# Kernel optimization log

Hardware: AMD Instinct MI355X
Metric: run time of the kernel (lower is better)

The kernel has to match this reference:

```python
import jax, jax.numpy as jnp
import numpy as np

S, B, D, H, DH = 1024, 4, 1024, 16, 64


def setup_inputs() -> dict:
    key = jax.random.key(0)
    ks = jax.random.split(key, 12)
    inp = {
        "query": jax.random.normal(ks[0], (S, B, D), dtype=jnp.float32),
        "key": jax.random.normal(ks[1], (S, B, D), dtype=jnp.float32),
        "value": jax.random.normal(ks[2], (S, B, D), dtype=jnp.float32),
        "key_mask": jax.random.randint(ks[3], (S, B), 0, 2, dtype=jnp.int32),
        # per-head stacked projection weights (original loops nn.Linear per head)
        "Wq": jax.random.normal(ks[4], (H, D, DH), dtype=jnp.float32) * 0.02,
        "bq": jnp.zeros((H, DH), dtype=jnp.float32),
        "Wk": jax.random.normal(ks[5], (H, D, DH), dtype=jnp.float32) * 0.02,
        "bk": jnp.zeros((H, DH), dtype=jnp.float32),
        "Wv": jax.random.normal(ks[6], (H, D, DH), dtype=jnp.float32) * 0.02,
        "bv": jnp.zeros((H, DH), dtype=jnp.float32),
        "Wo": jax.random.normal(ks[7], (H * DH, D), dtype=jnp.float32) * 0.02,
        "bo": jnp.zeros((D,), dtype=jnp.float32),
    }
    return inp


def reference(query, key, value, key_mask, Wq, bq, Wk, bk, Wv, bv, Wo, bo):
    # query/key/value: [S, B, D] (seq-major, matching torch einsum 'imk,jmk->imj')
    q = jnp.einsum('smd,hdk->smhk', query, Wq) + bq  # [Sq, B, H, DH]
    k = jnp.einsum('smd,hdk->smhk', key, Wk) + bk    # [Sk, B, H, DH]
    v = jnp.einsum('smd,hdk->smhk', value, Wv) + bv  # [Sk, B, H, DH]

    scale = 1.0 / jnp.sqrt(jnp.float32(DH))
    scores = jnp.einsum('imhk,jmhk->himj', q, k) * scale  # [H, Sq, B, Sk]
    # key_mask: [Sk, B] -> transpose -> [B, Sk]; additive -1e18 masking
    scores = scores - key_mask.astype(jnp.float32).T * 1e18
    attn = jax.nn.softmax(scores, axis=-1)
    out = jnp.einsum('himj,jmhk->imhk', attn, v)  # [Sq, B, H, DH]
    concat = out.reshape(out.shape[0], out.shape[1], H * DH)
    return concat @ Wo + bo  # [Sq, B, D]
```

## Files before the change

kernel.cpp:

```cpp
#include <hip/hip_runtime.h>
#include <hip/hip_bf16.h>


typedef __attribute__((ext_vector_type(8))) short short8;
typedef __attribute__((ext_vector_type(4))) short short4_;
typedef __attribute__((ext_vector_type(4))) float f32x4;
typedef __attribute__((ext_vector_type(16))) float f32x16;
typedef __attribute__((ext_vector_type(8))) __bf16 bf16x8;
typedef __attribute__((ext_vector_type(4))) __bf16 bf16x4;

union B8 {
    short8 s;
    bf16x8 b;
    unsigned short u[8];
};
union B4 {
    short4_ s;
    bf16x4 b;
    unsigned short u[4];
    int i[2];
};

#if __has_builtin(__builtin_amdgcn_exp2f)
#define EXP2(x) __builtin_amdgcn_exp2f(x)
#else
#define EXP2(x) exp2f(x)
#endif
#if __has_builtin(__builtin_amdgcn_rcpf)
#define RCP(x) __builtin_amdgcn_rcpf(x)
#else
#define RCP(x) (1.0f / (x))
#endif

static __device__ __forceinline__ unsigned short f2bf_rne(float f) {
    union { float f; unsigned u; } v; v.f = f;
    unsigned r = v.u + 0x7FFFu + ((v.u >> 16) & 1u);
    return (unsigned short)(r >> 16);
}

static __device__ __forceinline__ void async_lds16(const void* g, const void* l) {
    __builtin_amdgcn_global_load_lds(
        (const __attribute__((address_space(1))) unsigned int*)(unsigned long long)g,
        (__attribute__((address_space(3))) unsigned int*)(unsigned int)(unsigned long long)l,
        16, 0, 0);
}

__global__ __launch_bounds__(256) void prep(
    const float* __restrict__ Wq, const float* __restrict__ Wk,
    const float* __restrict__ Wv, const float* __restrict__ Wo,
    const float* __restrict__ query, const float* __restrict__ key,
    const float* __restrict__ value,
    unsigned short* __restrict__ WT,
    unsigned short* __restrict__ qA, unsigned short* __restrict__ kA,
    unsigned short* __restrict__ vA) {
    const int t = threadIdx.x;
    const int z = blockIdx.z;

    if (z >= 4) {
        const int zz = z - 4;
        const int tensor = zz >> 2;
        const int part = zz & 3;
        const float* src = (tensor == 0) ? query : (tensor == 1) ? key : value;
        unsigned short* dst = (tensor == 0) ? qA : (tensor == 1) ? kA : vA;
        const int blk = blockIdx.y * 16 + blockIdx.x;
        const size_t base = (size_t)part * 1048576 + (size_t)blk * 4096 + t * 16;
        B8 w0, w1;
#pragma unroll
        for (int i = 0; i < 2; ++i) {
            f32x4 a = *(const f32x4*)(src + base + i * 8);
            f32x4 b = *(const f32x4*)(src + base + i * 8 + 4);
#pragma unroll
            for (int j = 0; j < 4; ++j) {
                (i ? w1 : w0).u[j] = f2bf_rne(a[j]);
                (i ? w1 : w0).u[4 + j] = f2bf_rne(b[j]);
            }
        }
        *(short8*)(dst + base) = w0.s;
        *(short8*)(dst + base + 8) = w1.s;
        return;
    }

    __shared__ float sT[64][65];
    const int dtile = blockIdx.x;
    const int sub = blockIdx.y;
    const float* src;
    int spitch;
    unsigned short* dst;
    if (z < 3) {
        const float* W = (z == 0) ? Wq : (z == 1) ? Wk : Wv;
        src = W + (size_t)sub * 65536 + (size_t)dtile * 64 * 64;
        spitch = 64;
        dst = WT + (size_t)z * 1048576 + (size_t)(sub * 64) * 1024 + dtile * 64;
    } else {
        src = Wo + (size_t)dtile * 64 * 1024 + sub * 64;
        spitch = 1024;
        dst = WT + (size_t)3 * 1048576 + (size_t)(sub * 64) * 1024 + dtile * 64;
    }

    const int r = t >> 2;
    const int cseg = (t & 3) * 16;
#pragma unroll
    for (int i = 0; i < 4; ++i) {
        f32x4 v = *(const f32x4*)(src + (size_t)r * spitch + cseg + i * 4);
#pragma unroll
        for (int j = 0; j < 4; ++j) sT[r][cseg + i * 4 + j] = v[j];
    }
    __syncthreads();
    B8 w0, w1;
#pragma unroll
    for (int i = 0; i < 8; ++i) {
        w0.u[i] = f2bf_rne(sT[cseg + i][r]);
        w1.u[i] = f2bf_rne(sT[cseg + 8 + i][r]);
    }
    *(short8*)(dst + (size_t)r * 1024 + cseg) = w0.s;
    *(short8*)(dst + (size_t)r * 1024 + cseg + 8) = w1.s;
}

template <bool OUT_F32, bool BIAS_ROW>
__device__ __forceinline__ void gemm128(unsigned short* __restrict__ sA,
                                        unsigned short* __restrict__ sB,
                                        const unsigned short* __restrict__ A,
                                        size_t lda,
                                        const unsigned short* __restrict__ Bt,
                                        size_t ldb,
                                        const float* __restrict__ bias,
                                        void* __restrict__ Cv, size_t ldc,
                                        float oscale, int row0, int col0) {
    const int t = threadIdx.x;
    const int w = t >> 6;
    const int lane = t & 63;
    const int quad = lane >> 4;
    const int l15 = lane & 15;
    const int l7 = l15 & 7;
    const int wr = w >> 1;
    const int wc = w & 1;
    const int lrow8 = lane >> 3;
    const int lseg = lane & 7;
    const int gseg = lseg ^ lrow8;

    f32x4 acc[4][4] = {};

    for (int k0 = 0; k0 < 1024; k0 += 64) {
#pragma unroll
        for (int i = 0; i < 4; ++i) {
            const int rr = w * 32 + i * 8;
            async_lds16(A + (size_t)(row0 + rr + lrow8) * lda + k0 + gseg * 8,
                        &sA[rr * 64]);
            async_lds16(Bt + (size_t)(col0 + rr + lrow8) * ldb + k0 + gseg * 8,
                        &sB[rr * 64]);
        }
        __syncthreads();
#pragma unroll
        for (int kf = 0; kf < 2; ++kf) {
            B8 af[4], bf[4];
#pragma unroll
            for (int i = 0; i < 4; ++i)
                af[i].s = *(const short8*)&sA[(wr * 64 + i * 16 + l15) * 64 +
                                              ((kf * 4 + quad) ^ l7) * 8];
#pragma unroll
            for (int j = 0; j < 4; ++j)
                bf[j].s = *(const short8*)&sB[(wc * 64 + j * 16 + l15) * 64 +
                                              ((kf * 4 + quad) ^ l7) * 8];
#pragma unroll
            for (int i = 0; i < 4; ++i)
#pragma unroll
                for (int j = 0; j < 4; ++j)
                    acc[i][j] = __builtin_amdgcn_mfma_f32_16x16x32_bf16(af[i].b, bf[j].b,
                                                                        acc[i][j], 0, 0, 0);
        }
        __syncthreads();
    }
    float brow[4][4];
    if constexpr (BIAS_ROW) {
#pragma unroll
        for (int i = 0; i < 4; ++i)
#pragma unroll
            for (int r = 0; r < 4; ++r)
                brow[i][r] = bias[row0 + wr * 64 + i * 16 + quad * 4 + r];
    }
#pragma unroll
    for (int j = 0; j < 4; ++j) {
        const int col = col0 + wc * 64 + j * 16 + l15;
        const float bcol = BIAS_ROW ? 0.0f : bias[col];
#pragma unroll
        for (int i = 0; i < 4; ++i) {
#pragma unroll
            for (int r = 0; r < 4; ++r) {
                const int row = row0 + wr * 64 + i * 16 + quad * 4 + r;
                const size_t idx = (size_t)row * ldc + col;
                const float bb = BIAS_ROW ? brow[i][r] : bcol;
                const float val = (acc[i][j][r] + bb) * oscale;
                if constexpr (OUT_F32)
                    ((float*)Cv)[idx] = val;
                else
                    ((unsigned short*)Cv)[idx] = f2bf_rne(val);
            }
        }
    }
}

#define SCALE_L2E 0.18033688011112042f

__global__ __launch_bounds__(256) void qkv_gemm(
    const unsigned short* __restrict__ qA, const unsigned short* __restrict__ kA,
    const unsigned short* __restrict__ vA,
    const unsigned short* __restrict__ WT,
    const float* __restrict__ bq, const float* __restrict__ bk, const float* __restrict__ bv,
    unsigned short* q_o, unsigned short* k_o, unsigned short* vT_o) {
    __shared__ unsigned short sA[128 * 64];
    __shared__ unsigned short sB[128 * 64];
    const int p = blockIdx.z;
    if (p < 2) {
        const unsigned short* A = (p == 0) ? qA : kA;
        const unsigned short* Bt = WT + (size_t)p * 1048576;
        const float* bias = (p == 0) ? bq : bk;
        unsigned short* C = (p == 0) ? q_o : k_o;
        const float osc = (p == 0) ? SCALE_L2E : 1.0f;
        gemm128<false, false>(sA, sB, A, 1024, Bt, 1024, bias, C, 1024, osc,
                              blockIdx.x * 128, blockIdx.y * 128);
    } else {
        const int b = blockIdx.x >> 3;
        const int rt = blockIdx.x & 7;
        gemm128<false, true>(sA, sB, WT + (size_t)2 * 1048576, 1024,
                             vA + (size_t)b * 1024, 4096, bv,
                             vT_o + (size_t)b * 1048576, 1024, 1.0f,
                             rt * 128, blockIdx.y * 128);
    }
}

__global__ __launch_bounds__(256) void out_gemm(const unsigned short* __restrict__ A,
                                                const unsigned short* __restrict__ WT,
                                                const float* __restrict__ bo,
                                                float* __restrict__ C) {
    __shared__ unsigned short sA[128 * 64];
    __shared__ unsigned short sB[128 * 64];
    gemm128<true, false>(sA, sB, A, 1024, WT + (size_t)3 * 1048576, 1024, bo, C, 1024,
                         1.0f, blockIdx.x * 128, blockIdx.y * 128);
}

#define TP 72

#if __has_builtin(__builtin_amdgcn_mfma_f32_32x32x8bf16_1k)
#define HAVE_X8 1
#endif

__global__ __launch_bounds__(256) void attn_kernel(
    const unsigned short* __restrict__ q,
    const unsigned short* __restrict__ k,
    const unsigned short* __restrict__ vT,
    const int* __restrict__ key_mask,
    unsigned short* __restrict__ o) {
    __shared__ unsigned short sK[2][64 * TP];
    __shared__ unsigned short sVt[2][64 * TP];
    __shared__ float sBias[1024];
    __shared__ unsigned long long sBits[16];

    const int t = threadIdx.x;
    const int wave = t >> 6;
    const int lane = t & 63;
    const int n31 = lane & 31;
    const int hh = lane >> 5;

    const int L = blockIdx.x + 8 * (blockIdx.y + 4 * blockIdx.z);
    const int xcd = L & 7;
    const int kk = L >> 3;
    const int g = (xcd << 3) | (kk >> 3);
    const int qt = kk & 7;
    const int b = g & 3;
    const int h = g >> 2;
    const int q0w = qt * 128 + wave * 32;

    const int srow = t >> 3;
    const int sseg = t & 7;

#pragma unroll
    for (int i = 0; i < 4; ++i) {
        const int idx = i * 4 + wave;
        const int sk = idx * 64 + lane;
        unsigned long long bal = __ballot(key_mask[sk * 4 + b] != 0);
        if (lane == 0) sBits[idx] = bal;
    }
    __syncthreads();
#pragma unroll
    for (int i = 0; i < 4; ++i) {
        const int idx = t * 4 + i;
        const int r = idx & 15;
        const int hb = (idx >> 4) & 1;
        const int blk = (idx >> 5) & 1;
        const int kt = idx >> 6;
        const int row = (r & 3) + 8 * (r >> 2) + 4 * hb + blk * 32;
        sBias[idx] = ((sBits[kt] >> row) & 1ull) ? -16384.0f : 0.0f;
    }

    bf16x8 qf[4];
    {
        const unsigned short* qrow =
            q + ((size_t)(q0w + n31) * 4 + b) * 1024 + h * 64 + hh * 8;
#pragma unroll
        for (int kc = 0; kc < 4; ++kc) {
            B8 tmp;
            tmp.s = *(const short8*)(qrow + kc * 16);
            qf[kc] = tmp.b;
        }
    }

    f32x16 O0 = {}, O1 = {}, L_ = {};
    B4 ones;
#pragma unroll
    for (int j = 0; j < 4; ++j) ones.u[j] = 0x3F80;
#if !defined(HAVE_X8)
    B8 ones8;
#pragma unroll
    for (int j = 0; j < 8; ++j) ones8.u[j] = 0x3F80;
#endif

    const unsigned short* kbase = k + (size_t)b * 1024 + h * 64;
    const unsigned short* vtb = vT + ((size_t)(b * 16 + h) * 64) * 1024;

    {
        const unsigned short* kr = kbase + (size_t)srow * 4096 + sseg * 8;
        short8 ka = *(const short8*)kr;
        short8 kb2 = *(const short8*)(kr + (size_t)32 * 4096);
        const unsigned short* vr = vtb + (size_t)srow * 1024 + sseg * 8;
        short8 va = *(const short8*)vr;
        short8 vb2 = *(const short8*)(vr + (size_t)32 * 1024);
        *(short8*)&sK[0][srow * TP + sseg * 8] = ka;
        *(short8*)&sK[0][(32 + srow) * TP + sseg * 8] = kb2;
        *(short8*)&sVt[0][srow * TP + sseg * 8] = va;
        *(short8*)&sVt[0][(32 + srow) * TP + sseg * 8] = vb2;
    }

#pragma unroll 2
    for (int kt = 0; kt < 16; ++kt) {
        const int cur = kt & 1;
        __syncthreads();
        short8 nka, nkb, nva, nvb;
        if (kt < 15) {
            const int k0n = (kt + 1) * 64;
            const unsigned short* kr = kbase + (size_t)(k0n + srow) * 4096 + sseg * 8;
            nka = *(const short8*)kr;
            nkb = *(const short8*)(kr + (size_t)32 * 4096);
            const unsigned short* vr = vtb + (size_t)srow * 1024 + k0n + sseg * 8;
            nva = *(const short8*)vr;
            nvb = *(const short8*)(vr + (size_t)32 * 1024);
        }
        B4 pfr[2][4];
#pragma unroll
        for (int blk = 0; blk < 2; ++blk) {
            f32x16 c;
            const f32x4* bp = (const f32x4*)&sBias[((kt * 2 + blk) * 2 + hh) * 16];
#pragma unroll
            for (int i = 0; i < 4; ++i) {
                f32x4 x = bp[i];
#pragma unroll
                for (int j = 0; j < 4; ++j) c[i * 4 + j] = x[j];
            }
            __builtin_amdgcn_s_setprio(1);
#pragma unroll
            for (int kc = 0; kc < 4; ++kc) {
                B8 af;
                af.s = *(const short8*)&sK[cur][(blk * 32 + n31) * TP + kc * 16 + hh * 8];
                c = __builtin_amdgcn_mfma_f32_32x32x16_bf16(af.b, qf[kc], c, 0, 0, 0);
            }
            __builtin_amdgcn_s_setprio(0);
#pragma unroll
            for (int gg = 0; gg < 4; ++gg)
#pragma unroll
                for (int j = 0; j < 4; ++j)
                    pfr[blk][gg].b[j] = (__bf16)EXP2(c[gg * 4 + j]);
        }
#if defined(HAVE_X8)
        __builtin_amdgcn_s_setprio(1);
#pragma unroll
        for (int blk = 0; blk < 2; ++blk) {
#pragma unroll
            for (int gg = 0; gg < 4; ++gg) {
                const int sko = blk * 32 + gg * 8 + hh * 4;
                B4 b0, b1;
                b0.s = *(const short4_*)&sVt[cur][n31 * TP + sko];
                b1.s = *(const short4_*)&sVt[cur][(32 + n31) * TP + sko];
                O0 = __builtin_amdgcn_mfma_f32_32x32x8bf16_1k(pfr[blk][gg].s, b0.s, O0, 0, 0, 0);
                O1 = __builtin_amdgcn_mfma_f32_32x32x8bf16_1k(pfr[blk][gg].s, b1.s, O1, 0, 0, 0);
                L_ = __builtin_amdgcn_mfma_f32_32x32x8bf16_1k(pfr[blk][gg].s, ones.s, L_, 0, 0, 0);
            }
        }
        __builtin_amdgcn_s_setprio(0);
#else
        __builtin_amdgcn_s_setprio(1);
#pragma unroll
        for (int blk = 0; blk < 2; ++blk) {
            B4 par[4];
#pragma unroll
            for (int gg = 0; gg < 4; ++gg) {
                par[gg].i[0] = __shfl_xor(pfr[blk][gg].i[0], 32);
                par[gg].i[1] = __shfl_xor(pfr[blk][gg].i[1], 32);
            }
#pragma unroll
            for (int w = 0; w < 2; ++w) {
                const int gsel = 2 * w + hh;
                B4 lo = (hh == 0) ? pfr[blk][gsel] : par[gsel];
                B4 hi = (hh == 0) ? par[gsel] : pfr[blk][gsel];
                B8 afr;
#pragma unroll
                for (int j = 0; j < 4; ++j) {
                    afr.u[j] = lo.u[j];
                    afr.u[4 + j] = hi.u[j];
                }
                const int sko = blk * 32 + w * 16 + hh * 8;
                B8 b0, b1;
                b0.s = *(const short8*)&sVt[cur][n31 * TP + sko];
                b1.s = *(const short8*)&sVt[cur][(32 + n31) * TP + sko];
                O0 = __builtin_amdgcn_mfma_f32_32x32x16_bf16(afr.b, b0.b, O0, 0, 0, 0);
                O1 = __builtin_amdgcn_mfma_f32_32x32x16_bf16(afr.b, b1.b, O1, 0, 0, 0);
                L_ = __builtin_amdgcn_mfma_f32_32x32x16_bf16(afr.b, ones8.b, L_, 0, 0, 0);
            }
        }
        __builtin_amdgcn_s_setprio(0);
#endif
        if (kt < 15) {
            const int nb = 1 - cur;
            *(short8*)&sK[nb][srow * TP + sseg * 8] = nka;
            *(short8*)&sK[nb][(32 + srow) * TP + sseg * 8] = nkb;
            *(short8*)&sVt[nb][srow * TP + sseg * 8] = nva;
            *(short8*)&sVt[nb][(32 + srow) * TP + sseg * 8] = nvb;
        }
    }

    unsigned short* obase = o + ((size_t)q0w * 4 + b) * 1024 + h * 64 + n31;
#pragma unroll
    for (int r = 0; r < 16; ++r) {
        const int qr = (r & 3) + 8 * (r >> 2) + 4 * hh;
        const float inv = RCP(L_[r]);
        obase[(size_t)qr * 4096] = f2bf_rne(O0[r] * inv);
        obase[(size_t)qr * 4096 + 32] = f2bf_rne(O1[r] * inv);
    }
}

extern "C" void kernel_launch(void* const* d_in, const int* in_sizes, int n_in,
                              void* d_out, int out_size, void* d_ws, size_t ws_size,
                              hipStream_t stream) {
    const float* query = (const float*)d_in[0];
    const float* key_ = (const float*)d_in[1];
    const float* value = (const float*)d_in[2];
    const int* key_mask = (const int*)d_in[3];
    const float* Wq = (const float*)d_in[4];
    const float* bq = (const float*)d_in[5];
    const float* Wk = (const float*)d_in[6];
    const float* bk = (const float*)d_in[7];
    const float* Wv = (const float*)d_in[8];
    const float* bv = (const float*)d_in[9];
    const float* Wo = (const float*)d_in[10];
    const float* bo = (const float*)d_in[11];
    float* out = (float*)d_out;

    const size_t NE = (size_t)4096 * 1024;
    unsigned short* q_ws = (unsigned short*)d_ws;
    unsigned short* k_ws = q_ws + NE;
    unsigned short* v_ws = k_ws + NE;
    unsigned short* a_ws = v_ws + NE;
    unsigned short* wt_ws = a_ws + NE;

    unsigned short* qA = a_ws;
    unsigned short* kA = (unsigned short*)d_out;
    unsigned short* vA = kA + NE;

    prep<<<dim3(16, 16, 16), 256, 0, stream>>>(Wq, Wk, Wv, Wo, query, key_, value,
                                               wt_ws, qA, kA, vA);
    qkv_gemm<<<dim3(32, 8, 3), 256, 0, stream>>>(qA, kA, vA, wt_ws,
                                                 bq, bk, bv, q_ws, k_ws, v_ws);
    attn_kernel<<<dim3(8, 4, 16), 256, 0, stream>>>(q_ws, k_ws, v_ws, key_mask, a_ws);
    out_gemm<<<dim3(32, 8, 1), 256, 0, stream>>>(a_ws, wt_ws, bo, out);
}
```

Baseline: 216.6 us.

## Double-buffer GEMM LDS tiles with BK=32 to overlap loads and MFMA

The shared GEMM routine now uses two LDS buffers with a K step of 32 instead of one buffer with a K step of 64. The next tile's async global-to-LDS loads are issued before the current tile is computed, and one barrier per iteration replaces two. The swizzle pattern is changed to match the narrower 32-element rows. The aim is to hide global load latency behind MFMA work in the QKV and output projections, at the cost of twice as many iterations, each with less compute, and more barriers overall.

```diff
diff --git a/kernel.cpp b/kernel.cpp
--- a/kernel.cpp
+++ b/kernel.cpp
@@ -131,45 +131,55 @@
     const int lane = t & 63;
     const int quad = lane >> 4;
     const int l15 = lane & 15;
-    const int l7 = l15 & 7;
     const int wr = w >> 1;
     const int wc = w & 1;
-    const int lrow8 = lane >> 3;
-    const int lseg = lane & 7;
-    const int gseg = lseg ^ lrow8;
+    const int srow16 = lane >> 2;
+    const int sgseg = (lane & 3) ^ ((lane >> 3) & 3);
+    const int rseg = (quad ^ ((l15 >> 1) & 3)) * 8;
 
     f32x4 acc[4][4] = {};
 
-    for (int k0 = 0; k0 < 1024; k0 += 64) {
-#pragma unroll
-        for (int i = 0; i < 4; ++i) {
-            const int rr = w * 32 + i * 8;
-            async_lds16(A + (size_t)(row0 + rr + lrow8) * lda + k0 + gseg * 8,
-                        &sA[rr * 64]);
-            async_lds16(Bt + (size_t)(col0 + rr + lrow8) * ldb + k0 + gseg * 8,
-                        &sB[rr * 64]);
-        }
+    const unsigned short* agp = A + (size_t)(row0 + w * 32 + srow16) * lda + sgseg * 8;
+    const unsigned short* agp2 = agp + (size_t)16 * lda;
+    const unsigned short* bgp = Bt + (size_t)(col0 + w * 32 + srow16) * ldb + sgseg * 8;
+    const unsigned short* bgp2 = bgp + (size_t)16 * ldb;
+    const int ldsA0 = (w * 32) * 32;
+    const int ldsA1 = (w * 32 + 16) * 32;
+
+    async_lds16(agp, sA + ldsA0);
+    async_lds16(agp2, sA + ldsA1);
+    async_lds16(bgp, sB + ldsA0);
+    async_lds16(bgp2, sB + ldsA1);
+
+#pragma unroll 2
+    for (int tt = 0; tt < 32; ++tt) {
+        const int cur = tt & 1;
         __syncthreads();
-#pragma unroll
-        for (int kf = 0; kf < 2; ++kf) {
-            B8 af[4], bf[4];
-#pragma unroll
-            for (int i = 0; i < 4; ++i)
-                af[i].s = *(const short8*)&sA[(wr * 64 + i * 16 + l15) * 64 +
-                                              ((kf * 4 + quad) ^ l7) * 8];
+        if (tt < 31) {
+            const int nb = cur ^ 1;
+            const int k0 = (tt + 1) * 32;
+            async_lds16(agp + k0, sA + nb * 4096 + ldsA0);
+            async_lds16(agp2 + k0, sA + nb * 4096 + ldsA1);
+            async_lds16(bgp + k0, sB + nb * 4096 + ldsA0);
+            async_lds16(bgp2 + k0, sB + nb * 4096 + ldsA1);
+        }
+        const unsigned short* sac = sA + cur * 4096;
+        const unsigned short* sbc = sB + cur * 4096;
+        B8 af[4], bf[4];
+#pragma unroll
+        for (int i = 0; i < 4; ++i)
+            af[i].s = *(const short8*)&sac[(wr * 64 + i * 16 + l15) * 32 + rseg];
+#pragma unroll
+        for (int j = 0; j < 4; ++j)
+            bf[j].s = *(const short8*)&sbc[(wc * 64 + j * 16 + l15) * 32 + rseg];
+#pragma unroll
+        for (int i = 0; i < 4; ++i)
 #pragma unroll
             for (int j = 0; j < 4; ++j)
-                bf[j].s = *(const short8*)&sB[(wc * 64 + j * 16 + l15) * 64 +
-                                              ((kf * 4 + quad) ^ l7) * 8];
-#pragma unroll
-            for (int i = 0; i < 4; ++i)
-#pragma unroll
-                for (int j = 0; j < 4; ++j)
-                    acc[i][j] = __builtin_amdgcn_mfma_f32_16x16x32_bf16(af[i].b, bf[j].b,
-                                                                        acc[i][j], 0, 0, 0);
-        }
-        __syncthreads();
-    }
+                acc[i][j] = __builtin_amdgcn_mfma_f32_16x16x32_bf16(af[i].b, bf[j].b,
+                                                                    acc[i][j], 0, 0, 0);
+    }
+
     float brow[4][4];
     if constexpr (BIAS_ROW) {
 #pragma unroll
@@ -207,8 +217,8 @@
     const unsigned short* __restrict__ WT,
     const float* __restrict__ bq, const float* __restrict__ bk, const float* __restrict__ bv,
     unsigned short* q_o, unsigned short* k_o, unsigned short* vT_o) {
-    __shared__ unsigned short sA[128 * 64];
-    __shared__ unsigned short sB[128 * 64];
+    __shared__ unsigned short sA[2 * 128 * 32];
+    __shared__ unsigned short sB[2 * 128 * 32];
     const int p = blockIdx.z;
     if (p < 2) {
         const unsigned short* A = (p == 0) ? qA : kA;
@@ -232,8 +242,8 @@
                                                 const unsigned short* __restrict__ WT,
                                                 const float* __restrict__ bo,
                                                 float* __restrict__ C) {
-    __shared__ unsigned short sA[128 * 64];
-    __shared__ unsigned short sB[128 * 64];
+    __shared__ unsigned short sA[2 * 128 * 32];
+    __shared__ unsigned short sB[2 * 128 * 32];
     gemm128<true, false>(sA, sB, A, 1024, WT + (size_t)3 * 1048576, 1024, bo, C, 1024,
                          1.0f, blockIdx.x * 128, blockIdx.y * 128);
 }
```

After: 213.9 us. About the same (-1.2%).
